# Optimization experiments

Measured on AMD Instinct MI355X. Metric: run time of the kernel, lower is better.

The kernel has to match this reference:

```python
import jax, jax.numpy as jnp
import numpy as np

B, S, T, E, H, F = 2, 2048, 2048, 1024, 16, 4096
HD = E // H
EPS = 1e-5


def setup_inputs() -> dict:
    key = jax.random.key(0)
    ks = jax.random.split(key, 16)
    def w(k, shape):
        return (jax.random.normal(k, shape, jnp.float32) * 0.02)
    d = {
        "x": jax.random.normal(ks[0], (B, S, E), jnp.float32),
        "enc": jax.random.normal(ks[1], (B, T, E), jnp.float32),
    }
    for i, n in enumerate(["sa_q", "sa_k", "sa_v", "sa_o", "ca_q", "ca_k", "ca_v", "ca_o"]):
        d[n + "w"] = w(ks[2 + i], (E, E))  # torch Linear: [out, in]
        d[n + "b"] = jnp.zeros((E,), jnp.float32)
    d["w1"] = w(ks[10], (F, E)); d["b1"] = jnp.zeros((F,), jnp.float32)
    d["w2"] = w(ks[11], (E, F)); d["b2"] = jnp.zeros((E,), jnp.float32)
    for n in ["ln1", "ln2", "ln3"]:
        d[n + "_g"] = jnp.ones((E,), jnp.float32)
        d[n + "_b"] = jnp.zeros((E,), jnp.float32)
    return d


def _layernorm(x, g, b):
    m = jnp.mean(x, axis=-1, keepdims=True)
    v = jnp.mean((x - m) ** 2, axis=-1, keepdims=True)
    return (x - m) / jnp.sqrt(v + EPS) * g + b


def _heads(x, w, b):
    bsz, sl, _ = x.shape
    y = x @ w.T + b
    return y.reshape(bsz, sl, H, HD).transpose(0, 2, 1, 3)  # [B,H,S,hd]


def _mha(xq, xkv, qw, qb, kw, kb, vw, vb, ow, ob, causal):
    q = _heads(xq, qw, qb)
    k = _heads(xkv, kw, kb)
    v = _heads(xkv, vw, vb)
    scores = jnp.einsum('bhsd,bhtd->bhst', q, k) / np.sqrt(HD).astype(np.float32)
    if causal:
        sl, tl = scores.shape[-2], scores.shape[-1]
        mask = jnp.tril(jnp.ones((sl, tl), bool))
        scores = jnp.where(mask, scores, -jnp.inf)
    a = jax.nn.softmax(scores, axis=-1)
    o = jnp.einsum('bhst,bhtd->bhsd', a, v)
    o = o.transpose(0, 2, 1, 3).reshape(xq.shape[0], xq.shape[1], E)
    return o @ ow.T + ob


def reference(x, enc,
              sa_qw, sa_qb, sa_kw, sa_kb, sa_vw, sa_vb, sa_ow, sa_ob,
              ca_qw, ca_qb, ca_kw, ca_kb, ca_vw, ca_vb, ca_ow, ca_ob,
              w1, b1, w2, b2,
              ln1_g, ln1_b, ln2_g, ln2_b, ln3_g, ln3_b):
    sa = _mha(x, x, sa_qw, sa_qb, sa_kw, sa_kb, sa_vw, sa_vb, sa_ow, sa_ob, True)
    x = _layernorm(x + sa, ln1_g, ln1_b)
    ca = _mha(x, enc, ca_qw, ca_qb, ca_kw, ca_kb, ca_vw, ca_vb, ca_ow, ca_ob, False)
    x = _layernorm(x + ca, ln2_g, ln2_b)
    ffn = jax.nn.relu(x @ w1.T + b1) @ w2.T + b2
    return _layernorm(x + ffn, ln3_g, ln3_b)
```

## Files before the change

### kernel.cpp

```cpp
#include <hip/hip_runtime.h>
#include <hip/hip_bf16.h>
#include <stdint.h>

typedef __attribute__((ext_vector_type(8))) short s16x8;
typedef __attribute__((ext_vector_type(4))) short s16x4;
typedef __attribute__((ext_vector_type(4))) float f32x4;

#define DEV static __device__ __forceinline__

DEV ushort f2bu(float f){
  unsigned u = __builtin_bit_cast(unsigned, f);
  return (ushort)((u + 0x7fffu + ((u >> 16) & 1u)) >> 16);
}
DEV ushort f2bn(float f){
  return __builtin_bit_cast(ushort, __float2bfloat16(f));
}

DEV void gload16(const void* g, void* l){
  __builtin_amdgcn_global_load_lds((const __attribute__((address_space(1))) void*)g,
                                   (__attribute__((address_space(3))) void*)l, 16, 0, 0);
}

#define SCALE_C 0.18033688f

struct ConvArgs {
  const float* src[17];
  void*        dst[17];
  int blk_end[17];
  int nel[17];
  unsigned f32mask;
};

__global__ void __launch_bounds__(256) k_conv(ConvArgs a){
  int bi = blockIdx.x, seg = 0;
  while (bi >= a.blk_end[seg]) seg++;
  int b0 = seg ? a.blk_end[seg-1] : 0;
  long off = (long)(bi - b0)*2048 + (long)threadIdx.x*8;
  if (off >= a.nel[seg]) return;
  const float* s = a.src[seg] + off;
  f32x4 v0 = *(const f32x4*)s;
  f32x4 v1 = *(const f32x4*)(s+4);
  if ((a.f32mask >> seg) & 1u){
    float* d = (float*)a.dst[seg] + off;
    *(f32x4*)d = v0; *(f32x4*)(d+4) = v1;
  } else {
    ushort* d = (ushort*)a.dst[seg] + off;
    s16x8 o;
#pragma unroll
    for (int j = 0; j < 4; j++){ o[j] = (short)f2bu(v0[j]); o[4+j] = (short)f2bu(v1[j]); }
    *(s16x8*)d = o;
  }
}

__global__ void __launch_bounds__(256) k_gemm(const ushort* __restrict__ A, const ushort* __restrict__ W,
    const float* __restrict__ bias, ushort* __restrict__ Cb,
    int M, int N, int K, int lda, int ldb, float scale)
{
  __shared__ __align__(16) ushort lsA[2][128*64];
  __shared__ __align__(16) ushort lsB[2][128*64];
  const int t = threadIdx.x, w = t >> 6, u = t & 63, lr = u & 15, lk = u >> 4;
  const int m0 = blockIdx.y * 128, n0 = blockIdx.x * 128;
  const int wm = w >> 1, wn = w & 1;
  const int rA = t >> 3, c8 = (t & 7) * 8;
  const ushort* Ap = A + (size_t)(m0 + rA) * lda + c8;
  const ushort* Wp = W + (size_t)(n0 + rA) * ldb + c8;
  f32x4 acc[4][4] = {};
  const int nk = K >> 6;

  auto stage = [&](int k0, int buf){
#pragma unroll
    for (int j = 0; j < 4; j++){
      gload16(Ap + (size_t)j*32*lda + k0, &lsA[buf][0] + j*2048 + w*512);
      gload16(Wp + (size_t)j*32*ldb + k0, &lsB[buf][0] + j*2048 + w*512);
    }
  };
  stage(0, 0);
  for (int tk = 0; tk < nk; ++tk){
    __syncthreads();
    if (tk + 1 < nk) stage((tk + 1) << 6, (tk + 1) & 1);
    const ushort* La = &lsA[tk & 1][0];
    const ushort* Lb = &lsB[tk & 1][0];
#pragma unroll
    for (int ks = 0; ks < 2; ks++){
      s16x8 af[4], bfr[4];
#pragma unroll
      for (int i = 0; i < 4; i++) af[i]  = *(const s16x8*)(La + (wm*64 + i*16 + lr)*64 + ks*32 + lk*8);
#pragma unroll
      for (int i = 0; i < 4; i++) bfr[i] = *(const s16x8*)(Lb + (wn*64 + i*16 + lr)*64 + ks*32 + lk*8);
#pragma unroll
      for (int mi = 0; mi < 4; mi++)
#pragma unroll
        for (int ni = 0; ni < 4; ni++)
          acc[mi][ni] = __builtin_amdgcn_mfma_f32_16x16x32_bf16(af[mi], bfr[ni], acc[mi][ni], 0, 0, 0);
    }
  }

#pragma unroll
  for (int mi = 0; mi < 4; mi++){
#pragma unroll
    for (int ni = 0; ni < 4; ni++){
      const int row = m0 + wm*64 + mi*16 + lk*4;
      const int col = n0 + wn*64 + ni*16 + lr;
      const float bv = bias[col];
#pragma unroll
      for (int i = 0; i < 4; i++){
        float v = (acc[mi][ni][i] + bv) * scale;
        Cb[(size_t)(row + i) * N + col] = f2bn(v);
      }
    }
  }
}

struct CfP { float* p[3]; };

template<int MODE>
__global__ void __launch_bounds__(512, 1) k_gemm256(const ushort* __restrict__ A, const ushort* __restrict__ W,
    const float* __restrict__ bias, CfP cf, ushort* __restrict__ Cb,
    int N, int Ktot, int lda, int ldb, int scaleLim, float scale)
{
  __shared__ __align__(16) ushort lsA[2][256*64];
  __shared__ __align__(16) ushort lsB[2][256*64];
  const int t = threadIdx.x, w = t >> 6, u = t & 63, lr = u & 15, lk = u >> 4;
  const int gx = gridDim.x;
  const int nwg = gx * gridDim.y;
  const int id = blockIdx.y * gx + blockIdx.x;
  const int swz = (id & 7) * (nwg >> 3) + (id >> 3);
  const int n0 = (swz % gx) * 256, m0 = (swz / gx) * 256;
  const int wm = w >> 2, wn = w & 3;
  const int s = blockIdx.z, NS = gridDim.z;
  const int ntT = Ktot >> 6;
  const int kb = (s * ntT) / NS;
  const int nt = ((s + 1) * ntT) / NS - kb;

  const int r0 = w*8 + (u >> 3), cc = u & 7;
  const int csw = 8 * (cc ^ (r0 & 7));
  const ushort* Ap = A + (size_t)(m0 + r0) * lda + csw + (size_t)kb * 64;
  const ushort* Wp = W + (size_t)(n0 + r0) * ldb + csw + (size_t)kb * 64;

  f32x4 acc[8][4] = {};
  const int swl = lr & 7;
  s16x8 afr[4], bfr[4];

#pragma unroll
  for (int j = 0; j < 4; j++){
    gload16(Ap + (size_t)(64*j)*lda, &lsA[0][0] + w*512 + j*4096);
    gload16(Wp + (size_t)(64*j)*ldb, &lsB[0][0] + w*512 + j*4096);
  }
  asm volatile("s_waitcnt vmcnt(0)" ::: "memory");
  __builtin_amdgcn_s_barrier();

  for (int tk = 0; tk < nt; ++tk){
    const char* La = (const char*)&lsA[tk & 1][0];
    const char* Lb = (const char*)&lsB[tk & 1][0];
    ushort* dA = &lsA[(tk & 1) ^ 1][0] + w*512;
    ushort* dB = &lsB[(tk & 1) ^ 1][0] + w*512;
    const bool pf = (tk + 1 < nt);
    const size_t k1 = (size_t)(tk + 1) << 6;

#pragma unroll
    for (int i = 0; i < 4; i++)
      afr[i] = *(const s16x8*)(La + (wm*128 + i*16 + lr)*128 + ((lk ^ swl) * 16));
#pragma unroll
    for (int i = 0; i < 4; i++)
      bfr[i] = *(const s16x8*)(Lb + (wn*64 + i*16 + lr)*128 + ((lk ^ swl) * 16));
    if (pf){
      gload16(Ap + k1, dA);
      gload16(Wp + k1, dB);
      gload16(Ap + (size_t)64*lda + k1, dA + 4096);
      gload16(Wp + (size_t)64*ldb + k1, dB + 4096);
    }
    __builtin_amdgcn_s_barrier();
    asm volatile("s_waitcnt lgkmcnt(0)" ::: "memory");
    __builtin_amdgcn_s_setprio(1);
#pragma unroll
    for (int mi = 0; mi < 4; mi++)
#pragma unroll
      for (int ni = 0; ni < 4; ni++)
        acc[mi][ni] = __builtin_amdgcn_mfma_f32_16x16x32_bf16(afr[mi], bfr[ni], acc[mi][ni], 0, 0, 0);
    __builtin_amdgcn_s_setprio(0);
    __builtin_amdgcn_s_barrier();

#pragma unroll
    for (int i = 0; i < 4; i++)
      afr[i] = *(const s16x8*)(La + (wm*128 + 64 + i*16 + lr)*128 + ((lk ^ swl) * 16));
    if (pf){
      gload16(Ap + (size_t)128*lda + k1, dA + 8192);
      gload16(Wp + (size_t)128*ldb + k1, dB + 8192);
      gload16(Ap + (size_t)192*lda + k1, dA + 12288);
      gload16(Wp + (size_t)192*ldb + k1, dB + 12288);
    }
    __builtin_amdgcn_s_barrier();
    asm volatile("s_waitcnt lgkmcnt(0)" ::: "memory");
    __builtin_amdgcn_s_setprio(1);
#pragma unroll
    for (int mi = 0; mi < 4; mi++)
#pragma unroll
      for (int ni = 0; ni < 4; ni++)
        acc[4+mi][ni] = __builtin_amdgcn_mfma_f32_16x16x32_bf16(afr[mi], bfr[ni], acc[4+mi][ni], 0, 0, 0);
    __builtin_amdgcn_s_setprio(0);
    __builtin_amdgcn_s_barrier();

#pragma unroll
    for (int i = 0; i < 4; i++)
      afr[i] = *(const s16x8*)(La + (wm*128 + i*16 + lr)*128 + (((4 + lk) ^ swl) * 16));
#pragma unroll
    for (int i = 0; i < 4; i++)
      bfr[i] = *(const s16x8*)(Lb + (wn*64 + i*16 + lr)*128 + (((4 + lk) ^ swl) * 16));
    __builtin_amdgcn_s_barrier();
    asm volatile("s_waitcnt lgkmcnt(0)" ::: "memory");
    __builtin_amdgcn_s_setprio(1);
#pragma unroll
    for (int mi = 0; mi < 4; mi++)
#pragma unroll
      for (int ni = 0; ni < 4; ni++)
        acc[mi][ni] = __builtin_amdgcn_mfma_f32_16x16x32_bf16(afr[mi], bfr[ni], acc[mi][ni], 0, 0, 0);
    __builtin_amdgcn_s_setprio(0);
    __builtin_amdgcn_s_barrier();

#pragma unroll
    for (int i = 0; i < 4; i++)
      afr[i] = *(const s16x8*)(La + (wm*128 + 64 + i*16 + lr)*128 + (((4 + lk) ^ swl) * 16));
    __builtin_amdgcn_s_barrier();
    asm volatile("s_waitcnt lgkmcnt(0)" ::: "memory");
    __builtin_amdgcn_s_setprio(1);
#pragma unroll
    for (int mi = 0; mi < 4; mi++)
#pragma unroll
      for (int ni = 0; ni < 4; ni++)
        acc[4+mi][ni] = __builtin_amdgcn_mfma_f32_16x16x32_bf16(afr[mi], bfr[ni], acc[4+mi][ni], 0, 0, 0);
    __builtin_amdgcn_s_setprio(0);
    asm volatile("s_waitcnt vmcnt(0)" ::: "memory");
    __builtin_amdgcn_s_barrier();
  }

  float* Cf = (MODE == 1) ? cf.p[s] : nullptr;
#pragma unroll
  for (int mi = 0; mi < 8; mi++){
#pragma unroll
    for (int ni = 0; ni < 4; ni++){
      const int row = m0 + wm*128 + mi*16 + lk*4;
      const int col = n0 + wn*64 + ni*16 + lr;
      const float bv = (s == 0) ? bias[col] : 0.f;
#pragma unroll
      for (int i = 0; i < 4; i++){
        float v = acc[mi][ni][i] + bv;
        if (MODE == 2) v = fmaxf(v, 0.f);
        if (MODE == 0 && col < scaleLim) v *= scale;
        size_t idx = (size_t)(row + i) * N + col;
        if (MODE == 1) Cf[idx] = v; else Cb[idx] = f2bn(v);
      }
    }
  }
}

__global__ void __launch_bounds__(256) k_vt(const ushort* __restrict__ V, ushort* __restrict__ Vt,
                                            int stride, int S)
{
  __shared__ ushort tile[64][72];
  const int st = blockIdx.x*64, h = blockIdx.y, b = blockIdx.z;
  const int r = threadIdx.x >> 3, c8 = (threadIdx.x & 7)*8;
#pragma unroll
  for (int j = 0; j < 2; j++){
    int s = r + j*32;
    s16x8 v = *(const s16x8*)(V + (size_t)(b*S + st + s)*stride + h*64 + c8);
    *(s16x8*)&tile[s][c8] = v;
  }
  __syncthreads();
#pragma unroll
  for (int j = 0; j < 2; j++){
    int d = r + j*32;
    s16x8 o;
#pragma unroll
    for (int e = 0; e < 8; e++) o[e] = tile[c8+e][d];
    *(s16x8*)(Vt + ((size_t)((b*16 + h)*64 + d))*S + st + c8) = o;
  }
}

template<bool CAUSAL>
__global__ void __launch_bounds__(512) k_attn(const ushort* __restrict__ Q, const ushort* __restrict__ Kg,
    const ushort* __restrict__ Vt, ushort* __restrict__ O, int sQ, int sK, int SQ, int SKV)
{
  __shared__ __align__(16) ushort Kl[2][64*64];
  __shared__ __align__(16) ushort Vl[2][64*64];
  __shared__ __align__(16) ushort Pl[8][16*64];
  const int t = threadIdx.x, w = t >> 6, u = t & 63, lr = u & 15, lk = u >> 4;
  const int hb = blockIdx.x;
  const int b = hb >> 4, h = hb & 15;
  const int srow = t >> 3, scol = t & 7;
  const size_t kvbase = (size_t)b * SKV;
  const size_t vtbase = (size_t)((b*16 + h)*64);
  char* Pc = (char*)&Pl[w][0];
  const int swzq = (lr & 7) << 4;

  auto stage = [&](int kt, int buf){
    gload16(Kg + (kvbase + kt*64 + srow)*sK + h*64 + 8*(scol ^ (srow & 7)), &Kl[buf][0] + w*512);
    gload16(Vt + (vtbase + srow)*SKV + kt*64 + 8*(scol ^ (srow & 7)), &Vl[buf][0] + w*512);
  };

  const int NREP = CAUSAL ? 2 : 1;
#pragma unroll 1
  for (int rep = 0; rep < NREP; rep++){
    const int qt = CAUSAL ? (rep ? (int)blockIdx.y : (int)(2*gridDim.y - 1 - blockIdx.y))
                          : (int)blockIdx.y;
    const int q0 = qt * 128;

    const ushort* qp = Q + (size_t)(b*SQ + q0 + w*16 + lr) * sQ + h*64 + lk*8;
    s16x8 qf0 = *(const s16x8*)qp;
    s16x8 qf1 = *(const s16x8*)(qp + 32);

    f32x4 oacc[4] = {};
    f32x4 lacc = {};
    const int nkt = CAUSAL ? (2*qt + 2) : (SKV >> 6);

    stage(0, 0);
    __syncthreads();

    for (int kt = 0; kt < nkt; kt++){
      const int buf = kt & 1;
      if (kt + 1 < nkt) stage(kt + 1, buf ^ 1);
      char* Kc = (char*)&Kl[buf][0];
      char* Vc = (char*)&Vl[buf][0];

      f32x4 sacc[4] = {};
      __builtin_amdgcn_s_setprio(1);
#pragma unroll
      for (int ks = 0; ks < 2; ks++){
        s16x8 qf = ks ? qf1 : qf0;
#pragma unroll
        for (int ni = 0; ni < 4; ni++){
          int key = ni*16 + lr;
          s16x8 kf = *(const s16x8*)(Kc + key*128 + ((ks*64 + lk*16) ^ ((key & 7) << 4)));
          sacc[ni] = __builtin_amdgcn_mfma_f32_16x16x32_bf16(kf, qf, sacc[ni], 0, 0, 0);
        }
      }
      __builtin_amdgcn_s_setprio(0);
      if (CAUSAL && kt >= 2*qt){
        const int koff = kt*64 - q0;
#pragma unroll
        for (int ni = 0; ni < 4; ni++)
#pragma unroll
          for (int i = 0; i < 4; i++)
            if (koff + 16*ni + lk*4 + i > w*16 + lr) sacc[ni][i] = -1e30f;
      }

#pragma unroll
      for (int ni = 0; ni < 4; ni++){
#pragma unroll
        for (int i = 0; i < 4; i++) sacc[ni][i] = __builtin_exp2f(sacc[ni][i]);
        lacc += sacc[ni];
      }

#pragma unroll
      for (int ni = 0; ni < 4; ni++){
        s16x4 pk;
#pragma unroll
        for (int i = 0; i < 4; i++) pk[i] = (short)f2bn(sacc[ni][i]);
        *(s16x4*)(Pc + lr*128 + ((32*ni + 8*lk) ^ swzq)) = pk;
      }

      __builtin_amdgcn_s_setprio(1);
#pragma unroll
      for (int ks = 0; ks < 2; ks++){
        s16x8 pf = *(const s16x8*)(Pc + lr*128 + ((ks*64 + lk*16) ^ swzq));
#pragma unroll
        for (int ni = 0; ni < 4; ni++){
          int d = ni*16 + lr;
          s16x8 vf = *(const s16x8*)(Vc + d*128 + ((ks*64 + lk*16) ^ ((d & 7) << 4)));
          oacc[ni] = __builtin_amdgcn_mfma_f32_16x16x32_bf16(pf, vf, oacc[ni], 0, 0, 0);
        }
      }
      __builtin_amdgcn_s_setprio(0);
      __syncthreads();
    }

    float lrun = lacc[0] + lacc[1] + lacc[2] + lacc[3];
    lrun += __shfl_xor(lrun, 16);
    lrun += __shfl_xor(lrun, 32);
    float il = 1.f / lrun;
    float invl[4];
#pragma unroll
    for (int i = 0; i < 4; i++) invl[i] = __shfl(il, lk*4 + i);
#pragma unroll
    for (int ni = 0; ni < 4; ni++)
#pragma unroll
      for (int i = 0; i < 4; i++)
        O[(size_t)(b*SQ + q0 + w*16 + lk*4 + i)*1024 + h*64 + ni*16 + lr] = f2bn(oacc[ni][i] * invl[i]);
  }
}

template<bool WB16>
__global__ void __launch_bounds__(256) k_ln(const float* __restrict__ R, const float* __restrict__ P,
    const float* __restrict__ P2, const float* __restrict__ P3,
    const float* __restrict__ G, const float* __restrict__ Bv,
    float* __restrict__ Of, ushort* __restrict__ Ob)
{
  const int row = blockIdx.x, t = threadIdx.x, w = t >> 6, u = t & 63;
  const size_t base = (size_t)row * 1024 + t * 4;
  f32x4 r = *(const f32x4*)(R + base);
  f32x4 p = *(const f32x4*)(P + base);
  f32x4 v = r + p;
  if (P2){ f32x4 p2 = *(const f32x4*)(P2 + base); v += p2; }
  if (P3){ f32x4 p3 = *(const f32x4*)(P3 + base); v += p3; }
  float s = 0.f, q = 0.f;
#pragma unroll
  for (int j = 0; j < 4; j++){ s += v[j]; q += v[j]*v[j]; }
#pragma unroll
  for (int md = 1; md < 64; md <<= 1){ s += __shfl_xor(s, md); q += __shfl_xor(q, md); }
  __shared__ float ps[4], pq[4];
  if (u == 0){ ps[w] = s; pq[w] = q; }
  __syncthreads();
  s = ps[0] + ps[1] + ps[2] + ps[3];
  q = pq[0] + pq[1] + pq[2] + pq[3];
  const float mean = s * (1.f/1024.f);
  const float var  = q * (1.f/1024.f) - mean*mean;
  const float rstd = rsqrtf(var + 1e-5f);
  f32x4 g4 = *(const f32x4*)(G  + t*4);
  f32x4 b4 = *(const f32x4*)(Bv + t*4);
  f32x4 o;
#pragma unroll
  for (int j = 0; j < 4; j++) o[j] = (v[j] - mean) * rstd * g4[j] + b4[j];
  *(f32x4*)(Of + base) = o;
  if (WB16){
    s16x4 ob;
#pragma unroll
    for (int j = 0; j < 4; j++) ob[j] = (short)f2bn(o[j]);
    *(s16x4*)(Ob + base) = ob;
  }
}

extern "C" void kernel_launch(void* const* d_in, const int* in_sizes, int n_in,
                              void* d_out, int out_size, void* d_ws, size_t ws_size,
                              hipStream_t stream)
{
  const float* x   = (const float*)d_in[0];
  const float* enc = (const float*)d_in[1];
  const float* aw[8]; const float* ab[8];
  for (int i = 0; i < 8; i++){ aw[i] = (const float*)d_in[2 + 2*i]; ab[i] = (const float*)d_in[3 + 2*i]; }
  const float* w1 = (const float*)d_in[18]; const float* b1 = (const float*)d_in[19];
  const float* w2 = (const float*)d_in[20]; const float* b2 = (const float*)d_in[21];
  const float* lg[3] = {(const float*)d_in[22], (const float*)d_in[24], (const float*)d_in[26]};
  const float* lb[3] = {(const float*)d_in[23], (const float*)d_in[25], (const float*)d_in[27]};
  float* out = (float*)d_out;

  const size_t MB = 1024ull * 1024ull;
  if (ws_size < 129 * MB) return;
  char* ws = (char*)d_ws;
  ushort* wqkv = (ushort*)(ws + 0*MB);
  ushort* wcq  = (ushort*)(ws + 6*MB);
  ushort* wkv  = (ushort*)(ws + 8*MB);
  ushort* wo1w = (ushort*)(ws + 12*MB);
  ushort* wo2w = (ushort*)(ws + 14*MB);
  ushort* w1b  = (ushort*)(ws + 16*MB);
  ushort* w2b  = (ushort*)(ws + 24*MB);
  ushort* xb   = (ushort*)(ws + 32*MB);
  ushort* encb = (ushort*)(ws + 40*MB);
  ushort* attb = (ushort*)(ws + 48*MB);
  float*  proj = (float*)(ws + 56*MB);
  float*  x1f  = (float*)(ws + 72*MB);
  ushort* xab  = (ushort*)(ws + 88*MB);
  ushort* QKVb    = (ushort*)(ws + 96*MB);
  ushort* Vt1     = (ushort*)(ws + 120*MB);
  ushort* crossQb = (ushort*)(ws + 96*MB);
  ushort* encKVb  = (ushort*)(ws + 104*MB);
  ushort* Vt2     = (ushort*)(ws + 120*MB);
  ushort* hb      = (ushort*)(ws + 96*MB);
  float*  pWO     = (float*)(ws + 96*MB);
  float*  pF1     = (float*)(ws + 0*MB);
  float*  pF2     = (float*)(ws + 32*MB);
  float*  bqkv = (float*)(ws + 128*MB);
  float*  bkv  = (float*)(ws + 128*MB + 16384);

  ConvArgs ca;
  const float* srcs[17] = { x, enc, aw[0], aw[1], aw[2], aw[3], aw[4], aw[5], aw[6], aw[7],
                            w1, w2, ab[0], ab[1], ab[2], ab[5], ab[6] };
  void* dsts[17] = { xb, encb, wqkv, wqkv + 1048576, wqkv + 2097152, wo1w, wcq, wkv, wkv + 1048576, wo2w,
                     w1b, w2b, bqkv, bqkv + 1024, bqkv + 2048, bkv, bkv + 1024 };
  int nels[17] = { 4194304, 4194304, 1048576, 1048576, 1048576, 1048576, 1048576, 1048576, 1048576, 1048576,
                   4194304, 4194304, 1024, 1024, 1024, 1024, 1024 };
  int acc_blk = 0;
  for (int i = 0; i < 17; i++){
    ca.src[i] = srcs[i]; ca.dst[i] = dsts[i]; ca.nel[i] = nels[i];
    acc_blk += (nels[i] + 2047) / 2048;
    ca.blk_end[i] = acc_blk;
  }
  ca.f32mask = 0x1F000u;
  k_conv<<<acc_blk, 256, 0, stream>>>(ca);

  CfP none = {};

  k_gemm256<0><<<dim3(12,16,1), 512, 0, stream>>>(xb, wqkv, bqkv, none, QKVb, 3072, 1024, 1024, 1024, 1024, SCALE_C);
  k_vt<<<dim3(32,16,2), 256, 0, stream>>>(QKVb + 2048, Vt1, 3072, 2048);
  k_attn<true><<<dim3(32,8), 512, 0, stream>>>(QKVb, QKVb + 1024, Vt1, attb, 3072, 3072, 2048, 2048);
  { CfP cp = { { proj, pWO, nullptr } };
    k_gemm256<1><<<dim3(4,16,2), 512, 0, stream>>>(attb, wo1w, ab[3], cp, nullptr, 1024, 1024, 1024, 1024, 0, 1.f); }
  k_ln<true><<<4096, 256, 0, stream>>>(x, proj, pWO, nullptr, lg[0], lb[0], x1f, xab);

  k_gemm<<<dim3(8,32), 256, 0, stream>>>(xab, wcq, ab[4], crossQb, 4096, 1024, 1024, 1024, 1024, SCALE_C);
  k_gemm256<0><<<dim3(8,16,1), 512, 0, stream>>>(encb, wkv, bkv, none, encKVb, 2048, 1024, 1024, 1024, 0, 1.f);
  k_vt<<<dim3(32,16,2), 256, 0, stream>>>(encKVb + 1024, Vt2, 2048, 2048);
  k_attn<false><<<dim3(32,16), 512, 0, stream>>>(crossQb, encKVb, Vt2, attb, 1024, 2048, 2048, 2048);
  { CfP cp = { { proj, pWO, nullptr } };
    k_gemm256<1><<<dim3(4,16,2), 512, 0, stream>>>(attb, wo2w, ab[7], cp, nullptr, 1024, 1024, 1024, 1024, 0, 1.f); }
  k_ln<true><<<4096, 256, 0, stream>>>(x1f, proj, pWO, nullptr, lg[1], lb[1], x1f, xab);

  k_gemm256<2><<<dim3(16,16,1), 512, 0, stream>>>(xab, w1b, b1, none, hb, 4096, 1024, 1024, 1024, 0, 1.f);
  { CfP cp = { { proj, pF1, pF2 } };
    k_gemm256<1><<<dim3(4,16,3), 512, 0, stream>>>(hb, w2b, b2, cp, nullptr, 1024, 4096, 4096, 4096, 0, 1.f); }
  k_ln<false><<<4096, 256, 0, stream>>>(x1f, proj, pF1, pF2, lg[2], lb[2], out, nullptr);
}
```

Before: 413.7 us.

## Use 128-key attention tiles and a new split-K 128x128 GEMM for output projections

The attention kernel now processes 128 keys per iteration, with larger K/V LDS buffers, so it runs half as many loop iterations and barriers. The P·V step is split into two halves that reuse the per-wave P buffer, and an occupancy hint is added to the launch bounds. The output-projection and FFN-down GEMMs move from the 256-tile split-K kernel to a new 128x128 split-K kernel with two K-splits, which launches more blocks for better CU occupancy. The FFN-down path drops from three partial sums to two, simplifying the layernorm. The new GEMM has no LDS swizzle, so it risks bank conflicts, and the larger attention tiles add register pressure.

```diff
diff --git a/kernel.cpp b/kernel.cpp
--- a/kernel.cpp
+++ b/kernel.cpp
@@ -111,11 +111,68 @@
   }
 }
 
-struct CfP { float* p[3]; };
+__global__ void __launch_bounds__(256) k_gemmS(const ushort* __restrict__ A, const ushort* __restrict__ W,
+    const float* __restrict__ bias, float* __restrict__ Cf,
+    int M, int N, int Kext, int lda, int ldb, long long sstride)
+{
+  __shared__ __align__(16) ushort lsA[2][128*64];
+  __shared__ __align__(16) ushort lsB[2][128*64];
+  const int t = threadIdx.x, w = t >> 6, u = t & 63, lr = u & 15, lk = u >> 4;
+  const int m0 = blockIdx.y * 128, n0 = blockIdx.x * 128;
+  const int s = blockIdx.z;
+  const int wm = w >> 1, wn = w & 1;
+  const int rA = t >> 3, c8 = (t & 7) * 8;
+  const ushort* Ap = A + (size_t)(m0 + rA) * lda + (size_t)s * Kext + c8;
+  const ushort* Wp = W + (size_t)(n0 + rA) * ldb + (size_t)s * Kext + c8;
+  if (s){ bias = nullptr; Cf += sstride; }
+  f32x4 acc[4][4] = {};
+  const int nk = Kext >> 6;
+
+  auto stage = [&](int k0, int buf){
+#pragma unroll
+    for (int j = 0; j < 4; j++){
+      gload16(Ap + (size_t)j*32*lda + k0, &lsA[buf][0] + j*2048 + w*512);
+      gload16(Wp + (size_t)j*32*ldb + k0, &lsB[buf][0] + j*2048 + w*512);
+    }
+  };
+  stage(0, 0);
+  for (int tk = 0; tk < nk; ++tk){
+    __syncthreads();
+    if (tk + 1 < nk) stage((tk + 1) << 6, (tk + 1) & 1);
+    const ushort* La = &lsA[tk & 1][0];
+    const ushort* Lb = &lsB[tk & 1][0];
+#pragma unroll
+    for (int ks = 0; ks < 2; ks++){
+      s16x8 af[4], bfr[4];
+#pragma unroll
+      for (int i = 0; i < 4; i++) af[i]  = *(const s16x8*)(La + (wm*64 + i*16 + lr)*64 + ks*32 + lk*8);
+#pragma unroll
+      for (int i = 0; i < 4; i++) bfr[i] = *(const s16x8*)(Lb + (wn*64 + i*16 + lr)*64 + ks*32 + lk*8);
+#pragma unroll
+      for (int mi = 0; mi < 4; mi++)
+#pragma unroll
+        for (int ni = 0; ni < 4; ni++)
+          acc[mi][ni] = __builtin_amdgcn_mfma_f32_16x16x32_bf16(af[mi], bfr[ni], acc[mi][ni], 0, 0, 0);
+    }
+  }
+
+#pragma unroll
+  for (int mi = 0; mi < 4; mi++){
+#pragma unroll
+    for (int ni = 0; ni < 4; ni++){
+      const int row = m0 + wm*64 + mi*16 + lk*4;
+      const int col = n0 + wn*64 + ni*16 + lr;
+      const float bv = bias ? bias[col] : 0.f;
+#pragma unroll
+      for (int i = 0; i < 4; i++)
+        Cf[(size_t)(row + i) * N + col] = acc[mi][ni][i] + bv;
+    }
+  }
+}
 
 template<int MODE>
 __global__ void __launch_bounds__(512, 1) k_gemm256(const ushort* __restrict__ A, const ushort* __restrict__ W,
-    const float* __restrict__ bias, CfP cf, ushort* __restrict__ Cb,
+    const float* __restrict__ bias, ushort* __restrict__ Cb,
     int N, int Ktot, int lda, int ldb, int scaleLim, float scale)
 {
   __shared__ __align__(16) ushort lsA[2][256*64];
@@ -127,15 +184,12 @@
   const int swz = (id & 7) * (nwg >> 3) + (id >> 3);
   const int n0 = (swz % gx) * 256, m0 = (swz / gx) * 256;
   const int wm = w >> 2, wn = w & 3;
-  const int s = blockIdx.z, NS = gridDim.z;
-  const int ntT = Ktot >> 6;
-  const int kb = (s * ntT) / NS;
-  const int nt = ((s + 1) * ntT) / NS - kb;
+  const int nt = Ktot >> 6;
 
   const int r0 = w*8 + (u >> 3), cc = u & 7;
   const int csw = 8 * (cc ^ (r0 & 7));
-  const ushort* Ap = A + (size_t)(m0 + r0) * lda + csw + (size_t)kb * 64;
-  const ushort* Wp = W + (size_t)(n0 + r0) * ldb + csw + (size_t)kb * 64;
+  const ushort* Ap = A + (size_t)(m0 + r0) * lda + csw;
+  const ushort* Wp = W + (size_t)(n0 + r0) * ldb + csw;
 
   f32x4 acc[8][4] = {};
   const int swl = lr & 7;
@@ -233,21 +287,19 @@
     __builtin_amdgcn_s_barrier();
   }
 
-  float* Cf = (MODE == 1) ? cf.p[s] : nullptr;
 #pragma unroll
   for (int mi = 0; mi < 8; mi++){
 #pragma unroll
     for (int ni = 0; ni < 4; ni++){
       const int row = m0 + wm*128 + mi*16 + lk*4;
       const int col = n0 + wn*64 + ni*16 + lr;
-      const float bv = (s == 0) ? bias[col] : 0.f;
+      const float bv = bias[col];
 #pragma unroll
       for (int i = 0; i < 4; i++){
         float v = acc[mi][ni][i] + bv;
         if (MODE == 2) v = fmaxf(v, 0.f);
         if (MODE == 0 && col < scaleLim) v *= scale;
-        size_t idx = (size_t)(row + i) * N + col;
-        if (MODE == 1) Cf[idx] = v; else Cb[idx] = f2bn(v);
+        Cb[(size_t)(row + i) * N + col] = f2bn(v);
       }
     }
   }
@@ -277,24 +329,32 @@
 }
 
 template<bool CAUSAL>
-__global__ void __launch_bounds__(512) k_attn(const ushort* __restrict__ Q, const ushort* __restrict__ Kg,
+__global__ void __launch_bounds__(512, 4) k_attn(const ushort* __restrict__ Q, const ushort* __restrict__ Kg,
     const ushort* __restrict__ Vt, ushort* __restrict__ O, int sQ, int sK, int SQ, int SKV)
 {
-  __shared__ __align__(16) ushort Kl[2][64*64];
-  __shared__ __align__(16) ushort Vl[2][64*64];
+  __shared__ __align__(16) ushort Kl[2][128*64];
+  __shared__ __align__(16) ushort Vl[2][64*128];
   __shared__ __align__(16) ushort Pl[8][16*64];
   const int t = threadIdx.x, w = t >> 6, u = t & 63, lr = u & 15, lk = u >> 4;
   const int hb = blockIdx.x;
   const int b = hb >> 4, h = hb & 15;
-  const int srow = t >> 3, scol = t & 7;
+  const int krow = t >> 3, kcol = t & 7;
+  const int vrow = t >> 4, vcol = t & 15;
   const size_t kvbase = (size_t)b * SKV;
   const size_t vtbase = (size_t)((b*16 + h)*64);
   char* Pc = (char*)&Pl[w][0];
   const int swzq = (lr & 7) << 4;
 
   auto stage = [&](int kt, int buf){
-    gload16(Kg + (kvbase + kt*64 + srow)*sK + h*64 + 8*(scol ^ (srow & 7)), &Kl[buf][0] + w*512);
-    gload16(Vt + (vtbase + srow)*SKV + kt*64 + 8*(scol ^ (srow & 7)), &Vl[buf][0] + w*512);
+#pragma unroll
+    for (int p = 0; p < 2; p++){
+      int row = krow + p*64;
+      gload16(Kg + (kvbase + kt*128 + row)*sK + h*64 + 8*(kcol ^ (row & 7)),
+              &Kl[buf][0] + t*8 + p*4096);
+      int d = vrow + p*32;
+      gload16(Vt + (vtbase + d)*SKV + kt*128 + 8*(vcol ^ (d & 7)),
+              &Vl[buf][0] + t*8 + p*4096);
+    }
   };
 
   const int NREP = CAUSAL ? 2 : 1;
@@ -310,7 +370,7 @@
 
     f32x4 oacc[4] = {};
     f32x4 lacc = {};
-    const int nkt = CAUSAL ? (2*qt + 2) : (SKV >> 6);
+    const int nkt = CAUSAL ? (qt + 1) : (SKV >> 7);
 
     stage(0, 0);
     __syncthreads();
@@ -321,55 +381,56 @@
       char* Kc = (char*)&Kl[buf][0];
       char* Vc = (char*)&Vl[buf][0];
 
-      f32x4 sacc[4] = {};
+      f32x4 sacc[8] = {};
       __builtin_amdgcn_s_setprio(1);
 #pragma unroll
       for (int ks = 0; ks < 2; ks++){
         s16x8 qf = ks ? qf1 : qf0;
 #pragma unroll
-        for (int ni = 0; ni < 4; ni++){
+        for (int ni = 0; ni < 8; ni++){
           int key = ni*16 + lr;
           s16x8 kf = *(const s16x8*)(Kc + key*128 + ((ks*64 + lk*16) ^ ((key & 7) << 4)));
           sacc[ni] = __builtin_amdgcn_mfma_f32_16x16x32_bf16(kf, qf, sacc[ni], 0, 0, 0);
         }
       }
       __builtin_amdgcn_s_setprio(0);
-      if (CAUSAL && kt >= 2*qt){
-        const int koff = kt*64 - q0;
-#pragma unroll
-        for (int ni = 0; ni < 4; ni++)
+      if (CAUSAL && kt == qt){
+#pragma unroll
+        for (int ni = 0; ni < 8; ni++)
 #pragma unroll
           for (int i = 0; i < 4; i++)
-            if (koff + 16*ni + lk*4 + i > w*16 + lr) sacc[ni][i] = -1e30f;
+            if (16*ni + lk*4 + i > w*16 + lr) sacc[ni][i] = -1e30f;
       }
 
 #pragma unroll
-      for (int ni = 0; ni < 4; ni++){
+      for (int ni = 0; ni < 8; ni++){
 #pragma unroll
         for (int i = 0; i < 4; i++) sacc[ni][i] = __builtin_exp2f(sacc[ni][i]);
         lacc += sacc[ni];
       }
 
 #pragma unroll
-      for (int ni = 0; ni < 4; ni++){
-        s16x4 pk;
-#pragma unroll
-        for (int i = 0; i < 4; i++) pk[i] = (short)f2bn(sacc[ni][i]);
-        *(s16x4*)(Pc + lr*128 + ((32*ni + 8*lk) ^ swzq)) = pk;
+      for (int hf = 0; hf < 2; hf++){
+#pragma unroll
+        for (int ni = 0; ni < 4; ni++){
+          s16x4 pk;
+#pragma unroll
+          for (int i = 0; i < 4; i++) pk[i] = (short)f2bn(sacc[hf*4 + ni][i]);
+          *(s16x4*)(Pc + lr*128 + ((32*ni + 8*lk) ^ swzq)) = pk;
+        }
+        __builtin_amdgcn_s_setprio(1);
+#pragma unroll
+        for (int ks = 0; ks < 2; ks++){
+          s16x8 pf = *(const s16x8*)(Pc + lr*128 + ((ks*64 + lk*16) ^ swzq));
+#pragma unroll
+          for (int ni = 0; ni < 4; ni++){
+            int d = ni*16 + lr;
+            s16x8 vf = *(const s16x8*)(Vc + d*256 + ((hf*128 + ks*64 + lk*16) ^ ((d & 7) << 4)));
+            oacc[ni] = __builtin_amdgcn_mfma_f32_16x16x32_bf16(pf, vf, oacc[ni], 0, 0, 0);
+          }
+        }
+        __builtin_amdgcn_s_setprio(0);
       }
-
-      __builtin_amdgcn_s_setprio(1);
-#pragma unroll
-      for (int ks = 0; ks < 2; ks++){
-        s16x8 pf = *(const s16x8*)(Pc + lr*128 + ((ks*64 + lk*16) ^ swzq));
-#pragma unroll
-        for (int ni = 0; ni < 4; ni++){
-          int d = ni*16 + lr;
-          s16x8 vf = *(const s16x8*)(Vc + d*128 + ((ks*64 + lk*16) ^ ((d & 7) << 4)));
-          oacc[ni] = __builtin_amdgcn_mfma_f32_16x16x32_bf16(pf, vf, oacc[ni], 0, 0, 0);
-        }
-      }
-      __builtin_amdgcn_s_setprio(0);
       __syncthreads();
     }
 
@@ -390,8 +451,7 @@
 
 template<bool WB16>
 __global__ void __launch_bounds__(256) k_ln(const float* __restrict__ R, const float* __restrict__ P,
-    const float* __restrict__ P2, const float* __restrict__ P3,
-    const float* __restrict__ G, const float* __restrict__ Bv,
+    const float* __restrict__ P2, const float* __restrict__ G, const float* __restrict__ Bv,
     float* __restrict__ Of, ushort* __restrict__ Ob)
 {
   const int row = blockIdx.x, t = threadIdx.x, w = t >> 6, u = t & 63;
@@ -400,7 +460,6 @@
   f32x4 p = *(const f32x4*)(P + base);
   f32x4 v = r + p;
   if (P2){ f32x4 p2 = *(const f32x4*)(P2 + base); v += p2; }
-  if (P3){ f32x4 p3 = *(const f32x4*)(P3 + base); v += p3; }
   float s = 0.f, q = 0.f;
 #pragma unroll
   for (int j = 0; j < 4; j++){ s += v[j]; q += v[j]*v[j]; }
@@ -465,10 +524,12 @@
   ushort* Vt2     = (ushort*)(ws + 120*MB);
   ushort* hb      = (ushort*)(ws + 96*MB);
   float*  pWO     = (float*)(ws + 96*MB);
-  float*  pF1     = (float*)(ws + 0*MB);
-  float*  pF2     = (float*)(ws + 32*MB);
+  float*  pFF     = (float*)(ws + 32*MB);
   float*  bqkv = (float*)(ws + 128*MB);
   float*  bkv  = (float*)(ws + 128*MB + 16384);
+
+  const long long ssWO  = ((long long)(96 - 56) * (long long)MB) / 4;
+  const long long ssFFN = ((long long)(32 - 56) * (long long)MB) / 4;
 
   ConvArgs ca;
   const float* srcs[17] = { x, enc, aw[0], aw[1], aw[2], aw[3], aw[4], aw[5], aw[6], aw[7],
@@ -486,25 +547,20 @@
   ca.f32mask = 0x1F000u;
   k_conv<<<acc_blk, 256, 0, stream>>>(ca);
 
-  CfP none = {};
-
-  k_gemm256<0><<<dim3(12,16,1), 512, 0, stream>>>(xb, wqkv, bqkv, none, QKVb, 3072, 1024, 1024, 1024, 1024, SCALE_C);
+  k_gemm256<0><<<dim3(12,16), 512, 0, stream>>>(xb, wqkv, bqkv, QKVb, 3072, 1024, 1024, 1024, 1024, SCALE_C);
   k_vt<<<dim3(32,16,2), 256, 0, stream>>>(QKVb + 2048, Vt1, 3072, 2048);
   k_attn<true><<<dim3(32,8), 512, 0, stream>>>(QKVb, QKVb + 1024, Vt1, attb, 3072, 3072, 2048, 2048);
-  { CfP cp = { { proj, pWO, nullptr } };
-    k_gemm256<1><<<dim3(4,16,2), 512, 0, stream>>>(attb, wo1w, ab[3], cp, nullptr, 1024, 1024, 1024, 1024, 0, 1.f); }
-  k_ln<true><<<4096, 256, 0, stream>>>(x, proj, pWO, nullptr, lg[0], lb[0], x1f, xab);
+  k_gemmS<<<dim3(8,32,2), 256, 0, stream>>>(attb, wo1w, ab[3], proj, 4096, 1024, 512, 1024, 1024, ssWO);
+  k_ln<true><<<4096, 256, 0, stream>>>(x, proj, pWO, lg[0], lb[0], x1f, xab);
 
   k_gemm<<<dim3(8,32), 256, 0, stream>>>(xab, wcq, ab[4], crossQb, 4096, 1024, 1024, 1024, 1024, SCALE_C);
-  k_gemm256<0><<<dim3(8,16,1), 512, 0, stream>>>(encb, wkv, bkv, none, encKVb, 2048, 1024, 1024, 1024, 0, 1.f);
+  k_gemm256<0><<<dim3(8,16), 512, 0, stream>>>(encb, wkv, bkv, encKVb, 2048, 1024, 1024, 1024, 0, 1.f);
   k_vt<<<dim3(32,16,2), 256, 0, stream>>>(encKVb + 1024, Vt2, 2048, 2048);
   k_attn<false><<<dim3(32,16), 512, 0, stream>>>(crossQb, encKVb, Vt2, attb, 1024, 2048, 2048, 2048);
-  { CfP cp = { { proj, pWO, nullptr } };
-    k_gemm256<1><<<dim3(4,16,2), 512, 0, stream>>>(attb, wo2w, ab[7], cp, nullptr, 1024, 1024, 1024, 1024, 0, 1.f); }
-  k_ln<true><<<4096, 256, 0, stream>>>(x1f, proj, pWO, nullptr, lg[1], lb[1], x1f, xab);
-
-  k_gemm256<2><<<dim3(16,16,1), 512, 0, stream>>>(xab, w1b, b1, none, hb, 4096, 1024, 1024, 1024, 0, 1.f);
-  { CfP cp = { { proj, pF1, pF2 } };
-    k_gemm256<1><<<dim3(4,16,3), 512, 0, stream>>>(hb, w2b, b2, cp, nullptr, 1024, 4096, 4096, 4096, 0, 1.f); }
-  k_ln<false><<<4096, 256, 0, stream>>>(x1f, proj, pF1, pF2, lg[2], lb[2], out, nullptr);
-}
+  k_gemmS<<<dim3(8,32,2), 256, 0, stream>>>(attb, wo2w, ab[7], proj, 4096, 1024, 512, 1024, 1024, ssWO);
+  k_ln<true><<<4096, 256, 0, stream>>>(x1f, proj, pWO, lg[1], lb[1], x1f, xab);
+
+  k_gemm256<2><<<dim3(16,16), 512, 0, stream>>>(xab, w1b, b1, hb, 4096, 1024, 1024, 1024, 0, 1.f);
+  k_gemmS<<<dim3(8,32,2), 256, 0, stream>>>(hb, w2b, b2, proj, 4096, 1024, 2048, 4096, 4096, ssFFN);
+  k_ln<false><<<4096, 256, 0, stream>>>(x1f, proj, pFF, lg[2], lb[2], out, nullptr);
+}
```

New measurement: 394.7 us. -4.6%, faster.
